# Kernel tuning notes

Measured on AMD Instinct MI355X. Metric: run time of the kernel, lower is better.

The kernel has to match this reference:

```python
import jax, jax.numpy as jnp
import numpy as np

EPS = 1e-5  # BatchNorm eps (torch default)

def setup_inputs() -> dict:
    key = jax.random.key(0)
    ks = jax.random.split(key, 12)
    B, C, H, W = 4, 256, 64, 64
    IC = 128  # inter_channels = C // 2
    s = 1.0 / np.sqrt(C)
    si = 1.0 / np.sqrt(IC)
    return {
        "x": jax.random.normal(ks[0], (B, C, H, W), jnp.float32),
        "y": jax.random.normal(ks[1], (B, C, H, W), jnp.float32),
        "g_w": jax.random.normal(ks[2], (IC, C), jnp.float32) * s,
        "g_b": jax.random.normal(ks[3], (IC,), jnp.float32) * 0.01,
        "dx_w": jax.random.normal(ks[4], (IC, C), jnp.float32) * s,
        "dx_b": jax.random.normal(ks[5], (IC,), jnp.float32) * 0.01,
        "dy_w": jax.random.normal(ks[6], (IC, C), jnp.float32) * s,
        "dy_b": jax.random.normal(ks[7], (IC,), jnp.float32) * 0.01,
        "w_w": jax.random.normal(ks[8], (C, IC), jnp.float32) * si,
        "w_b": jax.random.normal(ks[9], (C,), jnp.float32) * 0.01,
        "bn_gamma": jax.random.normal(ks[10], (C,), jnp.float32),
        "bn_beta": jax.random.normal(ks[11], (C,), jnp.float32) * 0.01,
    }

def _conv1x1(t, w, b):
    # t: [B,C,H,W], w: [O,C], b: [O] -> [B,O,H,W]
    return jnp.einsum('bchw,oc->bohw', t, w) + b[None, :, None, None]

def reference(x, y, g_w, g_b, dx_w, dx_b, dy_w, dy_b, w_w, w_b, bn_gamma, bn_beta):
    B, C, H, W = x.shape
    IC = g_w.shape[0]
    N = H * W
    g_y = _conv1x1(y, g_w, g_b).reshape(B, IC, N).transpose(0, 2, 1)      # [B,N,IC]
    theta_x = _conv1x1(x, dx_w, dx_b).reshape(B, IC, N).transpose(0, 2, 1)  # [B,N,IC]
    phi_y = _conv1x1(y, dy_w, dy_b).reshape(B, IC, N)                      # [B,IC,N]
    f = jnp.einsum('bnc,bcm->bnm', theta_x, phi_y)                         # [B,N,N]
    f_div_C = jax.nn.softmax(f, axis=-1)
    y2 = jnp.einsum('bnm,bmc->bnc', f_div_C, g_y)                          # [B,N,IC]
    y2 = y2.transpose(0, 2, 1).reshape(B, IC, H, W)
    wy = _conv1x1(y2, w_w, w_b)                                            # [B,C,H,W]
    # BatchNorm2d in training mode: batch stats over (B,H,W) per channel
    mean = jnp.mean(wy, axis=(0, 2, 3), keepdims=True)
    var = jnp.var(wy, axis=(0, 2, 3), keepdims=True)
    wy_bn = (wy - mean) / jnp.sqrt(var + EPS)
    wy_bn = wy_bn * bn_gamma[None, :, None, None] + bn_beta[None, :, None, None]
    return wy_bn + x
```

## Files before the change

### kernel.cpp

```cpp
#include <hip/hip_runtime.h>
#include <hip/hip_bf16.h>
#include <math.h>

typedef unsigned short ushort_t;
typedef __attribute__((ext_vector_type(8))) short     short8;
typedef __attribute__((ext_vector_type(8))) _Float16  half8;
typedef __attribute__((ext_vector_type(8))) unsigned short ushort8;
typedef __attribute__((ext_vector_type(4))) float     float4v;

__device__ __forceinline__ float b2f(ushort_t u) {
    return __uint_as_float(((unsigned)u) << 16);
}
__device__ __forceinline__ ushort_t f2b(float f) {
    unsigned i = __float_as_uint(f);
    return (ushort_t)((i + 0x7FFFu + ((i >> 16) & 1u)) >> 16);
}
__device__ __forceinline__ void split2(float v, ushort_t& h, ushort_t& l) {
    h = f2b(v);
    l = f2b(v - b2f(h));
}
__device__ __forceinline__ void glds16(const ushort_t* g, ushort_t* l) {
    __builtin_amdgcn_global_load_lds((const __attribute__((address_space(1))) void*)g,
                                     (__attribute__((address_space(3))) void*)l, 16, 0, 0);
}

#define WTFH_OFF   0
#define WTFL_OFF   196608
#define WWBH_OFF   393216
#define WWBL_OFF   458752
#define BIAS_OFF   524288
#define STATS_OFF  526336
#define PROJF_OFF  1048576
#define GT_OFF     9437184
#define OPART_OFF  13631488
#define WY_OFF     1048576

__global__ void prep_k(const float* __restrict__ dx_w, const float* __restrict__ dy_w,
                       const float* __restrict__ g_w,  const float* __restrict__ dx_b,
                       const float* __restrict__ dy_b, const float* __restrict__ g_b,
                       const float* __restrict__ w_w,
                       ushort_t* __restrict__ wtfh, ushort_t* __restrict__ wtfl,
                       ushort_t* __restrict__ wwbh, ushort_t* __restrict__ wwbl,
                       float* __restrict__ bias, float* __restrict__ stats) {
    int idx = blockIdx.x * 256 + threadIdx.x;
    int j = idx & 7, lane = (idx >> 3) & 63, kk = (idx >> 9) & 7, ot = idx >> 12;
    int o = ot * 16 + (lane & 15);
    int c = kk * 32 + ((lane >> 4) * 8) + j;
    float v;
    if (o < 128)      v = dx_w[o * 256 + c];
    else if (o < 256) v = dy_w[(o - 128) * 256 + c];
    else              v = g_w[(o - 256) * 256 + c];
    ushort_t h, l;
    split2(v, h, l);
    wtfh[idx] = h; wtfl[idx] = l;
    if (idx < 32768) {
        split2(w_w[idx], h, l);
        wwbh[idx] = h; wwbl[idx] = l;
    }
    if (idx < 384) {
        bias[idx] = (idx < 128) ? dx_b[idx]
                  : (idx < 256) ? dy_b[idx - 128]
                                : g_b[idx - 256];
    }
    if (idx < 512) stats[idx] = 0.f;
}

__global__ __launch_bounds__(256) void proj_k(const float* __restrict__ x,
                                              const float* __restrict__ y,
                                              const ushort_t* __restrict__ wtfh,
                                              const ushort_t* __restrict__ wtfl,
                                              const float* __restrict__ bias,
                                              ushort_t* __restrict__ projf,
                                              ushort_t* __restrict__ gT) {
    __shared__ ushort_t xT[2][32 * 256];
    int b = blockIdx.y, n0 = blockIdx.x * 32, z = blockIdx.z;
    int tid = threadIdx.x;
    int w = tid >> 6, lane = tid & 63;
    int mrow = lane & 15, quad = lane >> 4, koff = quad * 8;
    int half = w & 1, sect = w >> 1;
    int arow = half * 16 + mrow;
    const float* src = z ? y : x;

    #pragma unroll
    for (int i = 0; i < 4; i++) {
        int ch = tid + i * 256;
        int c = ch >> 2, off = (ch & 3) * 8;
        const float* p = src + (size_t)(b * 256 + c) * 4096 + n0 + off;
        float4v v0 = *(const float4v*)p;
        float4v v1 = *(const float4v*)(p + 4);
        #pragma unroll
        for (int jj = 0; jj < 4; jj++) {
            ushort_t h, l;
            split2(v0[jj], h, l);
            xT[0][(off + jj) * 256 + c] = h;
            xT[1][(off + jj) * 256 + c] = l;
            split2(v1[jj], h, l);
            xT[0][(off + 4 + jj) * 256 + c] = h;
            xT[1][(off + 4 + jj) * 256 + c] = l;
        }
    }
    __syncthreads();

    short8 fh[8], fl[8];
    #pragma unroll
    for (int kk = 0; kk < 8; kk++) {
        fh[kk] = *(const short8*)&xT[0][arow * 256 + kk * 32 + koff];
        fl[kk] = *(const short8*)&xT[1][arow * 256 + kk * 32 + koff];
    }

    int ot0 = z * 8 + sect * 4;
    for (int ot = ot0; ot < ot0 + 4; ot++) {
        float4v acc = {0.f, 0.f, 0.f, 0.f};
        #pragma unroll
        for (int kk = 0; kk < 8; kk++) {
            short8 bh = *(const short8*)(wtfh + (size_t)((ot * 8 + kk) * 64 + lane) * 8);
            short8 bl = *(const short8*)(wtfl + (size_t)((ot * 8 + kk) * 64 + lane) * 8);
            acc = __builtin_amdgcn_mfma_f32_16x16x32_bf16(fh[kk], bh, acc, 0, 0, 0);
            acc = __builtin_amdgcn_mfma_f32_16x16x32_bf16(fh[kk], bl, acc, 0, 0, 0);
            acc = __builtin_amdgcn_mfma_f32_16x16x32_bf16(fl[kk], bh, acc, 0, 0, 0);
        }
        int o = ot * 16 + mrow;
        float bo = bias[o];
        #pragma unroll
        for (int r = 0; r < 4; r++) {
            int n = n0 + half * 16 + quad * 4 + r;
            float v = acc[r] + bo;
            if (z < 2) {
                _Float16 hf = (_Float16)v;
                projf[(size_t)(b * 4096 + n) * 256 + o] = *(ushort_t*)&hf;
            } else {
                gT[(size_t)(b * 128 + (o - 256)) * 4096 + n] = f2b(v);
            }
        }
    }
}

__global__ __launch_bounds__(512, 2) void flash_k(const ushort_t* __restrict__ projf,
                                                  const ushort_t* __restrict__ gT,
                                                  float* __restrict__ opart,
                                                  float* __restrict__ oml,
                                                  int kqlog) {
    __shared__ __align__(16) ushort_t KsF[2][8192];
    __shared__ __align__(16) ushort_t VsF[2][8192];
    __shared__ __align__(16) ushort_t Ps[256 * 72];

    int b = blockIdx.y;
    int kq = blockIdx.x & ((1 << kqlog) - 1);
    int q0 = (blockIdx.x >> kqlog) * 256;
    int iters = 64 >> kqlog;
    int kt0 = kq * iters;
    int tid = threadIdx.x, w = tid >> 6, lane = tid & 63;
    int mrow = lane & 15, quad = lane >> 4, koff = quad * 8;

    int kRow[2], kCol[2], vIc[2], vOf[2], dstB[2];
    #pragma unroll
    for (int i = 0; i < 2; i++) {
        int ck = tid + i * 512, combo = ck >> 6, l2 = ck & 63;
        kRow[i] = (combo >> 2) * 16 + (l2 & 15);
        kCol[i] = 128 + (combo & 3) * 32 + (l2 >> 4) * 8;
        vIc[i]  = (combo >> 1) * 16 + (l2 & 15);
        vOf[i]  = (combo & 1) * 32 + (l2 >> 4) * 8;
        dstB[i] = (i * 512 + w * 64) * 8;
    }

    half8 qf[2][4];
    #pragma unroll
    for (int s = 0; s < 2; s++)
        #pragma unroll
        for (int kk = 0; kk < 4; kk++)
            qf[s][kk] = *(const half8*)(projf + (size_t)(b * 4096 + q0 + w * 32 + s * 16 + mrow) * 256
                                        + kk * 32 + koff);

    float4v oacc[2][8], oaccL[2];
    #pragma unroll
    for (int s = 0; s < 2; s++) {
        oaccL[s] = (float4v){0.f, 0.f, 0.f, 0.f};
        #pragma unroll
        for (int ot = 0; ot < 8; ot++) oacc[s][ot] = (float4v){0.f, 0.f, 0.f, 0.f};
    }
    short8 vones;
    #pragma unroll
    for (int j = 0; j < 8; j++) vones[j] = (short)0x3F80;

    {
        int kb = kt0 * 64;
        #pragma unroll
        for (int i = 0; i < 2; i++) {
            glds16(projf + (size_t)(b * 4096 + kb + kRow[i]) * 256 + kCol[i], &KsF[0][dstB[i]]);
            glds16(gT + (size_t)(b * 128 + vIc[i]) * 4096 + kb + vOf[i], &VsF[0][dstB[i]]);
        }
    }

    for (int kt = kt0; kt < kt0 + iters; kt++) {
        int cur = (kt - kt0) & 1;
        __syncthreads();
        if (kt + 1 < kt0 + iters) {
            int kb = (kt + 1) * 64;
            #pragma unroll
            for (int i = 0; i < 2; i++) {
                glds16(projf + (size_t)(b * 4096 + kb + kRow[i]) * 256 + kCol[i], &KsF[1 - cur][dstB[i]]);
                glds16(gT + (size_t)(b * 128 + vIc[i]) * 4096 + kb + vOf[i], &VsF[1 - cur][dstB[i]]);
            }
        }

        float4v sacc[2][4];
        #pragma unroll
        for (int ct = 0; ct < 4; ct++) {
            float4v a0 = {0.f, 0.f, 0.f, 0.f}, a1 = {0.f, 0.f, 0.f, 0.f};
            #pragma unroll
            for (int kk = 0; kk < 4; kk++) {
                half8 bh = *(const half8*)&KsF[cur][((ct * 4 + kk) * 64 + lane) * 8];
                a0 = __builtin_amdgcn_mfma_f32_16x16x32_f16(qf[0][kk], bh, a0, 0, 0, 0);
                a1 = __builtin_amdgcn_mfma_f32_16x16x32_f16(qf[1][kk], bh, a1, 0, 0, 0);
            }
            sacc[0][ct] = a0; sacc[1][ct] = a1;
        }

        #pragma unroll
        for (int s = 0; s < 2; s++)
            #pragma unroll
            for (int r = 0; r < 4; r++) {
                int prow = w * 32 + s * 16 + quad * 4 + r;
                #pragma unroll
                for (int ct = 0; ct < 4; ct++) {
                    float p = __builtin_exp2f(fmaf(sacc[s][ct][r], 1.44269504f, -92.332481f));
                    Ps[prow * 72 + ct * 16 + mrow] = f2b(p);
                }
            }
        __builtin_amdgcn_s_waitcnt(0xC07F);

        #pragma unroll
        for (int k2 = 0; k2 < 2; k2++) {
            short8 a0 = *(const short8*)&Ps[(w * 32 + mrow) * 72 + k2 * 32 + koff];
            short8 a1 = *(const short8*)&Ps[(w * 32 + 16 + mrow) * 72 + k2 * 32 + koff];
            #pragma unroll
            for (int ot = 0; ot < 8; ot++) {
                short8 bfr = *(const short8*)&VsF[cur][((ot * 2 + k2) * 64 + lane) * 8];
                oacc[0][ot] = __builtin_amdgcn_mfma_f32_16x16x32_bf16(a0, bfr, oacc[0][ot], 0, 0, 0);
                oacc[1][ot] = __builtin_amdgcn_mfma_f32_16x16x32_bf16(a1, bfr, oacc[1][ot], 0, 0, 0);
            }
            oaccL[0] = __builtin_amdgcn_mfma_f32_16x16x32_bf16(a0, vones, oaccL[0], 0, 0, 0);
            oaccL[1] = __builtin_amdgcn_mfma_f32_16x16x32_bf16(a1, vones, oaccL[1], 0, 0, 0);
        }
    }

    #pragma unroll
    for (int s = 0; s < 2; s++)
        #pragma unroll
        for (int ot = 0; ot < 8; ot++)
            #pragma unroll
            for (int r = 0; r < 4; r++) {
                int R = b * 4096 + q0 + w * 32 + s * 16 + quad * 4 + r;
                opart[((size_t)kq * 16384 + R) * 128 + ot * 16 + mrow] = oacc[s][ot][r];
            }
    if (mrow == 0) {
        #pragma unroll
        for (int s = 0; s < 2; s++)
            #pragma unroll
            for (int r = 0; r < 4; r++) {
                int R = b * 4096 + q0 + w * 32 + s * 16 + quad * 4 + r;
                oml[kq * 16384 + R] = oaccL[s][r];
            }
    }
}

__global__ __launch_bounds__(256) void wy_k(const float* __restrict__ opart,
                                            const float* __restrict__ oml,
                                            const ushort_t* __restrict__ wwbh,
                                            const ushort_t* __restrict__ wwbl,
                                            const float* __restrict__ w_b,
                                            ushort_t* __restrict__ wy,
                                            float* __restrict__ stats, int KQ) {
    __shared__ float s_sum[256], s_sq[256];
    int b = blockIdx.y, n0 = blockIdx.x * 32;
    int tid = threadIdx.x, w = tid >> 6, lane = tid & 63;
    s_sum[tid] = 0.f; s_sq[tid] = 0.f;
    __syncthreads();
    int mrow = lane & 15, quad = lane >> 4, koff = quad * 8;
    int half = w & 1, sect = w >> 1;
    int Rn = b * 4096 + n0 + half * 16 + mrow;

    float L = 0.f;
    for (int kq = 0; kq < KQ; kq++) L += oml[kq * 16384 + Rn];
    float invL = 1.f / L;

    short8 bfh[4], bfl[4];
    #pragma unroll
    for (int kk = 0; kk < 4; kk++) {
        float a[8];
        #pragma unroll
        for (int j = 0; j < 8; j++) a[j] = 0.f;
        for (int kq = 0; kq < KQ; kq++) {
            const float* p = opart + ((size_t)kq * 16384 + Rn) * 128 + kk * 32 + koff;
            float4v v0 = *(const float4v*)p;
            float4v v1 = *(const float4v*)(p + 4);
            #pragma unroll
            for (int j = 0; j < 4; j++) { a[j] += v0[j]; a[4 + j] += v1[j]; }
        }
        #pragma unroll
        for (int j = 0; j < 8; j++) {
            ushort_t h, l;
            split2(a[j] * invL, h, l);
            bfh[kk][j] = (short)h; bfl[kk][j] = (short)l;
        }
    }

    int coln = n0 + half * 16 + mrow;
    for (int cot = sect * 8; cot < sect * 8 + 8; cot++) {
        float4v acc = {0.f, 0.f, 0.f, 0.f};
        #pragma unroll
        for (int kk = 0; kk < 4; kk++) {
            size_t woff = (size_t)(cot * 16 + mrow) * 128 + kk * 32 + koff;
            short8 ah = *(const short8*)(wwbh + woff);
            short8 al = *(const short8*)(wwbl + woff);
            acc = __builtin_amdgcn_mfma_f32_16x16x32_bf16(ah, bfh[kk], acc, 0, 0, 0);
            acc = __builtin_amdgcn_mfma_f32_16x16x32_bf16(ah, bfl[kk], acc, 0, 0, 0);
            acc = __builtin_amdgcn_mfma_f32_16x16x32_bf16(al, bfh[kk], acc, 0, 0, 0);
        }
        #pragma unroll
        for (int r = 0; r < 4; r++) {
            int co = cot * 16 + quad * 4 + r;
            float v = acc[r] + w_b[co];
            wy[(size_t)(b * 256 + co) * 4096 + coln] = f2b(v);
            float sv = v, sq = v * v;
            #pragma unroll
            for (int d = 1; d < 16; d <<= 1) {
                sv += __shfl_xor(sv, d, 64);
                sq += __shfl_xor(sq, d, 64);
            }
            if (mrow == 0) { atomicAdd(&s_sum[co], sv); atomicAdd(&s_sq[co], sq); }
        }
    }
    __syncthreads();
    atomicAdd(&stats[tid], s_sum[tid]);
    atomicAdd(&stats[256 + tid], s_sq[tid]);
}

__global__ __launch_bounds__(256) void bn_k(const ushort_t* __restrict__ wy,
                                            const float* __restrict__ x,
                                            const float* __restrict__ gamma,
                                            const float* __restrict__ beta,
                                            const float* __restrict__ stats,
                                            float* __restrict__ out) {
    int idx = (blockIdx.x * 256 + threadIdx.x) * 8;
    int c = (idx >> 12) & 255;
    const float inv_cnt = 1.f / 16384.f;
    float mean = stats[c] * inv_cnt;
    float var  = stats[256 + c] * inv_cnt - mean * mean;
    float inv  = rsqrtf(var + 1e-5f);
    float scale = gamma[c] * inv;
    float shift = beta[c] - mean * scale;
    ushort8 wv = *(const ushort8*)(wy + idx);
    float4v x0 = *(const float4v*)(x + idx);
    float4v x1 = *(const float4v*)(x + idx + 4);
    float4v o0, o1;
    #pragma unroll
    for (int j = 0; j < 4; j++) {
        o0[j] = b2f(wv[j]) * scale + shift + x0[j];
        o1[j] = b2f(wv[4 + j]) * scale + shift + x1[j];
    }
    *(float4v*)(out + idx) = o0;
    *(float4v*)(out + idx + 4) = o1;
}

extern "C" void kernel_launch(void* const* d_in, const int* in_sizes, int n_in,
                              void* d_out, int out_size, void* d_ws, size_t ws_size,
                              hipStream_t stream) {
    const float* x    = (const float*)d_in[0];
    const float* y    = (const float*)d_in[1];
    const float* g_w  = (const float*)d_in[2];
    const float* g_b  = (const float*)d_in[3];
    const float* dx_w = (const float*)d_in[4];
    const float* dx_b = (const float*)d_in[5];
    const float* dy_w = (const float*)d_in[6];
    const float* dy_b = (const float*)d_in[7];
    const float* w_w  = (const float*)d_in[8];
    const float* w_b  = (const float*)d_in[9];
    const float* bn_g = (const float*)d_in[10];
    const float* bn_b = (const float*)d_in[11];

    char* ws = (char*)d_ws;
    ushort_t* wtfh  = (ushort_t*)(ws + WTFH_OFF);
    ushort_t* wtfl  = (ushort_t*)(ws + WTFL_OFF);
    ushort_t* wwbh  = (ushort_t*)(ws + WWBH_OFF);
    ushort_t* wwbl  = (ushort_t*)(ws + WWBL_OFF);
    float*    bias  = (float*)(ws + BIAS_OFF);
    float*    stats = (float*)(ws + STATS_OFF);
    ushort_t* projf = (ushort_t*)(ws + PROJF_OFF);
    ushort_t* gT    = (ushort_t*)(ws + GT_OFF);
    float*    opart = (float*)(ws + OPART_OFF);
    ushort_t* wy    = (ushort_t*)(ws + WY_OFF);
    float*    out   = (float*)d_out;

    int kqlog;
    if      (ws_size >= 13631488u + 4u * (8388608u + 65536u)) kqlog = 2;
    else if (ws_size >= 13631488u + 2u * (8388608u + 65536u)) kqlog = 1;
    else                                                      kqlog = 0;
    int KQ = 1 << kqlog;
    float* oml = (float*)(ws + OPART_OFF + (size_t)KQ * 8388608u);

    prep_k<<<384, 256, 0, stream>>>(dx_w, dy_w, g_w, dx_b, dy_b, g_b, w_w,
                                    wtfh, wtfl, wwbh, wwbl, bias, stats);
    proj_k<<<dim3(128, 4, 3), 256, 0, stream>>>(x, y, wtfh, wtfl, bias, projf, gT);
    flash_k<<<dim3(16 << kqlog, 4), 512, 0, stream>>>(projf, gT, opart, oml, kqlog);
    wy_k<<<dim3(128, 4), 256, 0, stream>>>(opart, oml, wwbh, wwbl, w_b, wy, stats, KQ);
    bn_k<<<2048, 256, 0, stream>>>(wy, x, bn_g, bn_b, stats, out);
}
```

Before: 226.0 us.

## Use single fp16 projection, bf16 partials, and 512-query flash tiles with more key splits

The projection GEMM now runs as a single fp16 MFMA instead of a three-pass bf16 hi/lo split. Flash attention handles 512 queries per block (64 per wave) with transposed MFMA operands and packed vector P stores. Partial outputs and row sums are stored as bf16 instead of fp32, and the key-split factor is doubled. Together these cut MFMA work, register-to-LDS traffic and partial-buffer bandwidth, at the cost of lower precision in the projections and partial sums and more register pressure per wave.

```diff
diff --git a/kernel.cpp b/kernel.cpp
--- a/kernel.cpp
+++ b/kernel.cpp
@@ -6,6 +6,7 @@
 typedef __attribute__((ext_vector_type(8))) short     short8;
 typedef __attribute__((ext_vector_type(8))) _Float16  half8;
 typedef __attribute__((ext_vector_type(8))) unsigned short ushort8;
+typedef __attribute__((ext_vector_type(4))) unsigned short ushort4v;
 typedef __attribute__((ext_vector_type(4))) float     float4v;
 
 __device__ __forceinline__ float b2f(ushort_t u) {
@@ -19,27 +20,30 @@
     h = f2b(v);
     l = f2b(v - b2f(h));
 }
+__device__ __forceinline__ ushort_t f2h(float v) {
+    _Float16 h = (_Float16)v;
+    return *(ushort_t*)&h;
+}
 __device__ __forceinline__ void glds16(const ushort_t* g, ushort_t* l) {
     __builtin_amdgcn_global_load_lds((const __attribute__((address_space(1))) void*)g,
                                      (__attribute__((address_space(3))) void*)l, 16, 0, 0);
 }
 
-#define WTFH_OFF   0
-#define WTFL_OFF   196608
-#define WWBH_OFF   393216
-#define WWBL_OFF   458752
-#define BIAS_OFF   524288
-#define STATS_OFF  526336
-#define PROJF_OFF  1048576
-#define GT_OFF     9437184
-#define OPART_OFF  13631488
-#define WY_OFF     1048576
+#define WTF_OFF    0
+#define WWBH_OFF   196608
+#define WWBL_OFF   262144
+#define BIAS_OFF   327680
+#define STATS_OFF  329216
+#define PROJF_OFF  393216
+#define GT_OFF     8781824
+#define OPART_OFF  12976128
+#define WY_OFF     393216
 
 __global__ void prep_k(const float* __restrict__ dx_w, const float* __restrict__ dy_w,
                        const float* __restrict__ g_w,  const float* __restrict__ dx_b,
                        const float* __restrict__ dy_b, const float* __restrict__ g_b,
                        const float* __restrict__ w_w,
-                       ushort_t* __restrict__ wtfh, ushort_t* __restrict__ wtfl,
+                       ushort_t* __restrict__ wtf,
                        ushort_t* __restrict__ wwbh, ushort_t* __restrict__ wwbl,
                        float* __restrict__ bias, float* __restrict__ stats) {
     int idx = blockIdx.x * 256 + threadIdx.x;
@@ -50,10 +54,9 @@
     if (o < 128)      v = dx_w[o * 256 + c];
     else if (o < 256) v = dy_w[(o - 128) * 256 + c];
     else              v = g_w[(o - 256) * 256 + c];
-    ushort_t h, l;
-    split2(v, h, l);
-    wtfh[idx] = h; wtfl[idx] = l;
+    wtf[idx] = f2h(v);
     if (idx < 32768) {
+        ushort_t h, l;
         split2(w_w[idx], h, l);
         wwbh[idx] = h; wwbl[idx] = l;
     }
@@ -67,12 +70,11 @@
 
 __global__ __launch_bounds__(256) void proj_k(const float* __restrict__ x,
                                               const float* __restrict__ y,
-                                              const ushort_t* __restrict__ wtfh,
-                                              const ushort_t* __restrict__ wtfl,
+                                              const ushort_t* __restrict__ wtf,
                                               const float* __restrict__ bias,
                                               ushort_t* __restrict__ projf,
                                               ushort_t* __restrict__ gT) {
-    __shared__ ushort_t xT[2][32 * 256];
+    __shared__ ushort_t xT[32 * 256];
     int b = blockIdx.y, n0 = blockIdx.x * 32, z = blockIdx.z;
     int tid = threadIdx.x;
     int w = tid >> 6, lane = tid & 63;
@@ -90,34 +92,24 @@
         float4v v1 = *(const float4v*)(p + 4);
         #pragma unroll
         for (int jj = 0; jj < 4; jj++) {
-            ushort_t h, l;
-            split2(v0[jj], h, l);
-            xT[0][(off + jj) * 256 + c] = h;
-            xT[1][(off + jj) * 256 + c] = l;
-            split2(v1[jj], h, l);
-            xT[0][(off + 4 + jj) * 256 + c] = h;
-            xT[1][(off + 4 + jj) * 256 + c] = l;
+            xT[(off + jj) * 256 + c]     = f2h(v0[jj]);
+            xT[(off + 4 + jj) * 256 + c] = f2h(v1[jj]);
         }
     }
     __syncthreads();
 
-    short8 fh[8], fl[8];
-    #pragma unroll
-    for (int kk = 0; kk < 8; kk++) {
-        fh[kk] = *(const short8*)&xT[0][arow * 256 + kk * 32 + koff];
-        fl[kk] = *(const short8*)&xT[1][arow * 256 + kk * 32 + koff];
-    }
+    half8 fx[8];
+    #pragma unroll
+    for (int kk = 0; kk < 8; kk++)
+        fx[kk] = *(const half8*)&xT[arow * 256 + kk * 32 + koff];
 
     int ot0 = z * 8 + sect * 4;
     for (int ot = ot0; ot < ot0 + 4; ot++) {
         float4v acc = {0.f, 0.f, 0.f, 0.f};
         #pragma unroll
         for (int kk = 0; kk < 8; kk++) {
-            short8 bh = *(const short8*)(wtfh + (size_t)((ot * 8 + kk) * 64 + lane) * 8);
-            short8 bl = *(const short8*)(wtfl + (size_t)((ot * 8 + kk) * 64 + lane) * 8);
-            acc = __builtin_amdgcn_mfma_f32_16x16x32_bf16(fh[kk], bh, acc, 0, 0, 0);
-            acc = __builtin_amdgcn_mfma_f32_16x16x32_bf16(fh[kk], bl, acc, 0, 0, 0);
-            acc = __builtin_amdgcn_mfma_f32_16x16x32_bf16(fl[kk], bh, acc, 0, 0, 0);
+            half8 bfr = *(const half8*)(wtf + (size_t)((ot * 8 + kk) * 64 + lane) * 8);
+            acc = __builtin_amdgcn_mfma_f32_16x16x32_f16(fx[kk], bfr, acc, 0, 0, 0);
         }
         int o = ot * 16 + mrow;
         float bo = bias[o];
@@ -125,28 +117,24 @@
         for (int r = 0; r < 4; r++) {
             int n = n0 + half * 16 + quad * 4 + r;
             float v = acc[r] + bo;
-            if (z < 2) {
-                _Float16 hf = (_Float16)v;
-                projf[(size_t)(b * 4096 + n) * 256 + o] = *(ushort_t*)&hf;
-            } else {
-                gT[(size_t)(b * 128 + (o - 256)) * 4096 + n] = f2b(v);
-            }
+            if (z < 2) projf[(size_t)(b * 4096 + n) * 256 + o] = f2h(v);
+            else       gT[(size_t)(b * 128 + (o - 256)) * 4096 + n] = f2b(v);
         }
     }
 }
 
 __global__ __launch_bounds__(512, 2) void flash_k(const ushort_t* __restrict__ projf,
                                                   const ushort_t* __restrict__ gT,
-                                                  float* __restrict__ opart,
-                                                  float* __restrict__ oml,
+                                                  ushort_t* __restrict__ opart,
+                                                  ushort_t* __restrict__ oml,
                                                   int kqlog) {
     __shared__ __align__(16) ushort_t KsF[2][8192];
     __shared__ __align__(16) ushort_t VsF[2][8192];
-    __shared__ __align__(16) ushort_t Ps[256 * 72];
+    __shared__ __align__(16) ushort_t Ps[512 * 72];
 
     int b = blockIdx.y;
     int kq = blockIdx.x & ((1 << kqlog) - 1);
-    int q0 = (blockIdx.x >> kqlog) * 256;
+    int q0 = (blockIdx.x >> kqlog) * 512;
     int iters = 64 >> kqlog;
     int kt0 = kq * iters;
     int tid = threadIdx.x, w = tid >> 6, lane = tid & 63;
@@ -163,17 +151,17 @@
         dstB[i] = (i * 512 + w * 64) * 8;
     }
 
-    half8 qf[2][4];
-    #pragma unroll
-    for (int s = 0; s < 2; s++)
+    half8 qf[4][4];
+    #pragma unroll
+    for (int s = 0; s < 4; s++)
         #pragma unroll
         for (int kk = 0; kk < 4; kk++)
-            qf[s][kk] = *(const half8*)(projf + (size_t)(b * 4096 + q0 + w * 32 + s * 16 + mrow) * 256
+            qf[s][kk] = *(const half8*)(projf + (size_t)(b * 4096 + q0 + w * 64 + s * 16 + mrow) * 256
                                         + kk * 32 + koff);
 
-    float4v oacc[2][8], oaccL[2];
-    #pragma unroll
-    for (int s = 0; s < 2; s++) {
+    float4v oacc[4][8], oaccL[4];
+    #pragma unroll
+    for (int s = 0; s < 4; s++) {
         oaccL[s] = (float4v){0.f, 0.f, 0.f, 0.f};
         #pragma unroll
         for (int ot = 0; ot < 8; ot++) oacc[s][ot] = (float4v){0.f, 0.f, 0.f, 0.f};
@@ -203,69 +191,64 @@
             }
         }
 
-        float4v sacc[2][4];
         #pragma unroll
         for (int ct = 0; ct < 4; ct++) {
-            float4v a0 = {0.f, 0.f, 0.f, 0.f}, a1 = {0.f, 0.f, 0.f, 0.f};
+            float4v sc[4];
+            #pragma unroll
+            for (int s = 0; s < 4; s++) sc[s] = (float4v){0.f, 0.f, 0.f, 0.f};
             #pragma unroll
             for (int kk = 0; kk < 4; kk++) {
-                half8 bh = *(const half8*)&KsF[cur][((ct * 4 + kk) * 64 + lane) * 8];
-                a0 = __builtin_amdgcn_mfma_f32_16x16x32_f16(qf[0][kk], bh, a0, 0, 0, 0);
-                a1 = __builtin_amdgcn_mfma_f32_16x16x32_f16(qf[1][kk], bh, a1, 0, 0, 0);
-            }
-            sacc[0][ct] = a0; sacc[1][ct] = a1;
-        }
-
-        #pragma unroll
-        for (int s = 0; s < 2; s++)
-            #pragma unroll
-            for (int r = 0; r < 4; r++) {
-                int prow = w * 32 + s * 16 + quad * 4 + r;
+                half8 ak = *(const half8*)&KsF[cur][((ct * 4 + kk) * 64 + lane) * 8];
                 #pragma unroll
-                for (int ct = 0; ct < 4; ct++) {
-                    float p = __builtin_exp2f(fmaf(sacc[s][ct][r], 1.44269504f, -92.332481f));
-                    Ps[prow * 72 + ct * 16 + mrow] = f2b(p);
-                }
-            }
+                for (int s = 0; s < 4; s++)
+                    sc[s] = __builtin_amdgcn_mfma_f32_16x16x32_f16(ak, qf[s][kk], sc[s], 0, 0, 0);
+            }
+            #pragma unroll
+            for (int s = 0; s < 4; s++) {
+                ushort4v pk;
+                #pragma unroll
+                for (int r = 0; r < 4; r++)
+                    pk[r] = f2b(__builtin_exp2f(fmaf(sc[s][r], 1.44269504f, -92.332481f)));
+                *(ushort4v*)&Ps[(w * 64 + s * 16 + mrow) * 72 + ct * 16 + quad * 4] = pk;
+            }
+        }
         __builtin_amdgcn_s_waitcnt(0xC07F);
 
         #pragma unroll
         for (int k2 = 0; k2 < 2; k2++) {
-            short8 a0 = *(const short8*)&Ps[(w * 32 + mrow) * 72 + k2 * 32 + koff];
-            short8 a1 = *(const short8*)&Ps[(w * 32 + 16 + mrow) * 72 + k2 * 32 + koff];
+            short8 bq[4];
+            #pragma unroll
+            for (int s = 0; s < 4; s++)
+                bq[s] = *(const short8*)&Ps[(w * 64 + s * 16 + mrow) * 72 + k2 * 32 + koff];
             #pragma unroll
             for (int ot = 0; ot < 8; ot++) {
-                short8 bfr = *(const short8*)&VsF[cur][((ot * 2 + k2) * 64 + lane) * 8];
-                oacc[0][ot] = __builtin_amdgcn_mfma_f32_16x16x32_bf16(a0, bfr, oacc[0][ot], 0, 0, 0);
-                oacc[1][ot] = __builtin_amdgcn_mfma_f32_16x16x32_bf16(a1, bfr, oacc[1][ot], 0, 0, 0);
-            }
-            oaccL[0] = __builtin_amdgcn_mfma_f32_16x16x32_bf16(a0, vones, oaccL[0], 0, 0, 0);
-            oaccL[1] = __builtin_amdgcn_mfma_f32_16x16x32_bf16(a1, vones, oaccL[1], 0, 0, 0);
-        }
-    }
-
-    #pragma unroll
-    for (int s = 0; s < 2; s++)
-        #pragma unroll
-        for (int ot = 0; ot < 8; ot++)
-            #pragma unroll
-            for (int r = 0; r < 4; r++) {
-                int R = b * 4096 + q0 + w * 32 + s * 16 + quad * 4 + r;
-                opart[((size_t)kq * 16384 + R) * 128 + ot * 16 + mrow] = oacc[s][ot][r];
-            }
-    if (mrow == 0) {
-        #pragma unroll
-        for (int s = 0; s < 2; s++)
-            #pragma unroll
-            for (int r = 0; r < 4; r++) {
-                int R = b * 4096 + q0 + w * 32 + s * 16 + quad * 4 + r;
-                oml[kq * 16384 + R] = oaccL[s][r];
-            }
-    }
-}
-
-__global__ __launch_bounds__(256) void wy_k(const float* __restrict__ opart,
-                                            const float* __restrict__ oml,
+                short8 av = *(const short8*)&VsF[cur][((ot * 2 + k2) * 64 + lane) * 8];
+                #pragma unroll
+                for (int s = 0; s < 4; s++)
+                    oacc[s][ot] = __builtin_amdgcn_mfma_f32_16x16x32_bf16(av, bq[s], oacc[s][ot], 0, 0, 0);
+            }
+            #pragma unroll
+            for (int s = 0; s < 4; s++)
+                oaccL[s] = __builtin_amdgcn_mfma_f32_16x16x32_bf16(vones, bq[s], oaccL[s], 0, 0, 0);
+        }
+    }
+
+    #pragma unroll
+    for (int s = 0; s < 4; s++) {
+        int R = b * 4096 + q0 + w * 64 + s * 16 + mrow;
+        #pragma unroll
+        for (int ot = 0; ot < 8; ot++) {
+            ushort4v ov;
+            #pragma unroll
+            for (int r = 0; r < 4; r++) ov[r] = f2b(oacc[s][ot][r]);
+            *(ushort4v*)(opart + ((size_t)kq * 16384 + R) * 128 + ot * 16 + quad * 4) = ov;
+        }
+        if (quad == 0) oml[kq * 16384 + R] = f2b(oaccL[s][0]);
+    }
+}
+
+__global__ __launch_bounds__(256) void wy_k(const ushort_t* __restrict__ opart,
+                                            const ushort_t* __restrict__ oml,
                                             const ushort_t* __restrict__ wwbh,
                                             const ushort_t* __restrict__ wwbl,
                                             const float* __restrict__ w_b,
@@ -281,7 +264,7 @@
     int Rn = b * 4096 + n0 + half * 16 + mrow;
 
     float L = 0.f;
-    for (int kq = 0; kq < KQ; kq++) L += oml[kq * 16384 + Rn];
+    for (int kq = 0; kq < KQ; kq++) L += b2f(oml[kq * 16384 + Rn]);
     float invL = 1.f / L;
 
     short8 bfh[4], bfl[4];
@@ -291,11 +274,9 @@
         #pragma unroll
         for (int j = 0; j < 8; j++) a[j] = 0.f;
         for (int kq = 0; kq < KQ; kq++) {
-            const float* p = opart + ((size_t)kq * 16384 + Rn) * 128 + kk * 32 + koff;
-            float4v v0 = *(const float4v*)p;
-            float4v v1 = *(const float4v*)(p + 4);
-            #pragma unroll
-            for (int j = 0; j < 4; j++) { a[j] += v0[j]; a[4 + j] += v1[j]; }
+            ushort8 v = *(const ushort8*)(opart + ((size_t)kq * 16384 + Rn) * 128 + kk * 32 + koff);
+            #pragma unroll
+            for (int j = 0; j < 8; j++) a[j] += b2f(v[j]);
         }
         #pragma unroll
         for (int j = 0; j < 8; j++) {
@@ -380,29 +361,28 @@
     const float* bn_b = (const float*)d_in[11];
 
     char* ws = (char*)d_ws;
-    ushort_t* wtfh  = (ushort_t*)(ws + WTFH_OFF);
-    ushort_t* wtfl  = (ushort_t*)(ws + WTFL_OFF);
+    ushort_t* wtf   = (ushort_t*)(ws + WTF_OFF);
     ushort_t* wwbh  = (ushort_t*)(ws + WWBH_OFF);
     ushort_t* wwbl  = (ushort_t*)(ws + WWBL_OFF);
     float*    bias  = (float*)(ws + BIAS_OFF);
     float*    stats = (float*)(ws + STATS_OFF);
     ushort_t* projf = (ushort_t*)(ws + PROJF_OFF);
     ushort_t* gT    = (ushort_t*)(ws + GT_OFF);
-    float*    opart = (float*)(ws + OPART_OFF);
+    ushort_t* opart = (ushort_t*)(ws + OPART_OFF);
     ushort_t* wy    = (ushort_t*)(ws + WY_OFF);
     float*    out   = (float*)d_out;
 
     int kqlog;
-    if      (ws_size >= 13631488u + 4u * (8388608u + 65536u)) kqlog = 2;
-    else if (ws_size >= 13631488u + 2u * (8388608u + 65536u)) kqlog = 1;
-    else                                                      kqlog = 0;
+    if      (ws_size >= 12976128u + 8u * (4194304u + 32768u)) kqlog = 3;
+    else if (ws_size >= 12976128u + 4u * (4194304u + 32768u)) kqlog = 2;
+    else                                                      kqlog = 1;
     int KQ = 1 << kqlog;
-    float* oml = (float*)(ws + OPART_OFF + (size_t)KQ * 8388608u);
+    ushort_t* oml = opart + (size_t)KQ * 2097152u;
 
     prep_k<<<384, 256, 0, stream>>>(dx_w, dy_w, g_w, dx_b, dy_b, g_b, w_w,
-                                    wtfh, wtfl, wwbh, wwbl, bias, stats);
-    proj_k<<<dim3(128, 4, 3), 256, 0, stream>>>(x, y, wtfh, wtfl, bias, projf, gT);
-    flash_k<<<dim3(16 << kqlog, 4), 512, 0, stream>>>(projf, gT, opart, oml, kqlog);
+                                    wtf, wwbh, wwbl, bias, stats);
+    proj_k<<<dim3(128, 4, 3), 256, 0, stream>>>(x, y, wtf, bias, projf, gT);
+    flash_k<<<dim3(8 << kqlog, 4), 512, 0, stream>>>(projf, gT, opart, oml, kqlog);
     wy_k<<<dim3(128, 4), 256, 0, stream>>>(opart, oml, wwbh, wwbl, w_b, wy, stats, KQ);
     bn_k<<<2048, 256, 0, stream>>>(wy, x, bn_g, bn_b, stats, out);
 }
```

After: 224.0 us. About the same (-0.9%).
